# Kernel tuning notes

Hardware: AMD Instinct MI355X
Metric: run time of the kernel (lower is better)

## Reference

```python
import jax, jax.numpy as jnp
import numpy as np
from jax import lax

B, N, F = 64, 768, 256
P, T, K = 64, 16, 3  # per_lead, after_lead, kernel_size


def setup_inputs() -> dict:
    key = jax.random.key(0)
    k1, k2, k3, k4, k5 = jax.random.split(key, 5)
    x = jax.random.normal(k1, (B, N, F), dtype=jnp.float32)
    adj = jax.random.uniform(k2, (B, N, N), dtype=jnp.float32)
    fan_in = P * 1 * K
    bound = 1.0 / np.sqrt(fan_in)
    conv_w = jax.random.uniform(k3, (T, P, 1, K), minval=-bound, maxval=bound, dtype=jnp.float32)
    conv_b = jax.random.uniform(k4, (T,), minval=-bound, maxval=bound, dtype=jnp.float32)
    re_param = jax.random.normal(k5, (K, 1), dtype=jnp.float32)
    return {"x": x, "adj": adj, "conv_w": conv_w, "conv_b": conv_b, "re_param": re_param}


def reference(x, adj, conv_w, conv_b, re_param):
    b, n, f = x.shape
    t, p, _, k = conv_w.shape
    L = n // p  # number of leads
    # feature pooling: [B, P, L, F] -conv(1,k)-> [B, T, L, F]
    x4 = x.reshape(b, p, L, f)
    pad = (k - 1) // 2
    y = lax.conv_general_dilated(
        x4, conv_w, window_strides=(1, 1), padding=[(0, 0), (pad, pad)],
        dimension_numbers=("NCHW", "OIHW", "NCHW"))
    y = y + conv_b[None, :, None, None]
    pooled_x = y.reshape(b, t * L, f)
    # assignment matrix s = conv_w @ re_param  -> [T, P]
    s = jnp.einsum("tpik,kj->tp", conv_w, re_param)
    # block-diagonal coarsening: for every (lead_i, lead_j) block do s @ A_ij @ s^T
    adj5 = adj.reshape(b, L, p, L, p)
    pooled = jnp.einsum("tp,blpmq,uq->bltmu", s, adj5, s)
    pooled_adj = pooled.reshape(b, L * t, L * t)
    return pooled_x, pooled_adj
```

## Files before the change

### kernel.cpp

```cpp
#include <hip/hip_runtime.h>

#define B_ 64
#define N_ 768
#define F_ 256
#define P_ 64
#define T_ 16
#define K_ 3
#define L_ 12
#define TSTR 772

__global__ __launch_bounds__(256) void fused_pool_kernel(
    const float* __restrict__ x, const float* __restrict__ adj,
    const float* __restrict__ conv_w, const float* __restrict__ conv_b,
    const float* __restrict__ re_param,
    float* __restrict__ out_x, float* __restrict__ out_adj)
{
    __shared__ float sT[P_][T_];
    __shared__ float tmp[T_][TSTR];

    const int g  = blockIdx.x;
    const int Lg = (g & 7) * 192 + (g >> 3);
    const int b  = Lg / 24;
    const int r  = Lg % 24;
    const int tid = threadIdx.x;

    if (r >= L_) {
        const int l = r - L_;
        const int f = tid;
        const float* xb = x + (size_t)b * N_ * F_ + (size_t)l * F_;

        float acc[T_];
        #pragma unroll
        for (int t = 0; t < T_; ++t) acc[t] = conv_b[t];

        for (int p0 = 0; p0 < P_; p0 += 2) {
            float xm[2], x0[2], xp[2];
            #pragma unroll
            for (int rr = 0; rr < 2; ++rr) {
                const float* row = xb + (size_t)(p0 + rr) * (L_ * F_);
                xm[rr] = (f > 0)      ? row[f - 1] : 0.f;
                x0[rr] = row[f];
                xp[rr] = (f < F_ - 1) ? row[f + 1] : 0.f;
            }
            #pragma unroll
            for (int rr = 0; rr < 2; ++rr) {
                const float* wp = conv_w + (p0 + rr) * K_;
                #pragma unroll
                for (int t = 0; t < T_; ++t) {
                    const float w0 = wp[t * (P_ * K_) + 0];
                    const float w1 = wp[t * (P_ * K_) + 1];
                    const float w2 = wp[t * (P_ * K_) + 2];
                    acc[t] = fmaf(xm[rr], w0, fmaf(x0[rr], w1, fmaf(xp[rr], w2, acc[t])));
                }
            }
        }
        float* ob = out_x + (size_t)b * (T_ * L_) * F_ + f;
        #pragma unroll
        for (int t = 0; t < T_; ++t)
            ob[(size_t)(t * L_ + l) * F_] = acc[t];
        return;
    }

    const int l = r;

    const float r0 = re_param[0], r1 = re_param[1], r2 = re_param[2];
    for (int j = tid; j < P_ * T_; j += 256) {
        const int p = j >> 4, t = j & 15;
        const float* wv = conv_w + (size_t)t * (P_ * K_) + (size_t)p * K_;
        sT[p][t] = wv[0] * r0 + wv[1] * r1 + wv[2] * r2;
    }
    __syncthreads();

    float acc[T_][3];
    #pragma unroll
    for (int t = 0; t < T_; ++t)
        #pragma unroll
        for (int c = 0; c < 3; ++c) acc[t][c] = 0.f;

    const float* ab = adj + (size_t)b * N_ * N_ + (size_t)(l * P_) * N_ + tid;
    for (int p0 = 0; p0 < P_; p0 += 8) {
        float a[8][3];
        #pragma unroll
        for (int rr = 0; rr < 8; ++rr) {
            const float* row = ab + (size_t)(p0 + rr) * N_;
            a[rr][0] = row[0];
            a[rr][1] = row[256];
            a[rr][2] = row[512];
        }
        #pragma unroll
        for (int rr = 0; rr < 8; ++rr) {
            #pragma unroll
            for (int j = 0; j < 4; ++j) {
                const float4 sv = *(const float4*)&sT[p0 + rr][4 * j];
                acc[4*j+0][0] = fmaf(sv.x, a[rr][0], acc[4*j+0][0]);
                acc[4*j+0][1] = fmaf(sv.x, a[rr][1], acc[4*j+0][1]);
                acc[4*j+0][2] = fmaf(sv.x, a[rr][2], acc[4*j+0][2]);
                acc[4*j+1][0] = fmaf(sv.y, a[rr][0], acc[4*j+1][0]);
                acc[4*j+1][1] = fmaf(sv.y, a[rr][1], acc[4*j+1][1]);
                acc[4*j+1][2] = fmaf(sv.y, a[rr][2], acc[4*j+1][2]);
                acc[4*j+2][0] = fmaf(sv.z, a[rr][0], acc[4*j+2][0]);
                acc[4*j+2][1] = fmaf(sv.z, a[rr][1], acc[4*j+2][1]);
                acc[4*j+2][2] = fmaf(sv.z, a[rr][2], acc[4*j+2][2]);
                acc[4*j+3][0] = fmaf(sv.w, a[rr][0], acc[4*j+3][0]);
                acc[4*j+3][1] = fmaf(sv.w, a[rr][1], acc[4*j+3][1]);
                acc[4*j+3][2] = fmaf(sv.w, a[rr][2], acc[4*j+3][2]);
            }
        }
    }
    #pragma unroll
    for (int t = 0; t < T_; ++t) {
        tmp[t][tid]       = acc[t][0];
        tmp[t][tid + 256] = acc[t][1];
        tmp[t][tid + 512] = acc[t][2];
    }
    __syncthreads();

    const int t = tid >> 4, u = tid & 15;
    float sum[L_];
    #pragma unroll
    for (int m = 0; m < L_; ++m) sum[m] = 0.f;

    for (int q4 = 0; q4 < P_; q4 += 4) {
        const float s0 = sT[q4 + 0][u];
        const float s1 = sT[q4 + 1][u];
        const float s2 = sT[q4 + 2][u];
        const float s3 = sT[q4 + 3][u];
        #pragma unroll
        for (int m = 0; m < L_; ++m) {
            const float4 tv = *(const float4*)&tmp[t][m * P_ + q4];
            sum[m] = fmaf(tv.x, s0, fmaf(tv.y, s1, fmaf(tv.z, s2, fmaf(tv.w, s3, sum[m]))));
        }
    }

    float* ob = out_adj + (size_t)b * (L_ * T_) * (L_ * T_)
                        + (size_t)(l * T_ + t) * (L_ * T_) + u;
    #pragma unroll
    for (int m = 0; m < L_; ++m)
        ob[m * T_] = sum[m];
}

extern "C" void kernel_launch(void* const* d_in, const int* in_sizes, int n_in,
                              void* d_out, int out_size, void* d_ws, size_t ws_size,
                              hipStream_t stream) {
    (void)in_sizes; (void)n_in; (void)out_size; (void)d_ws; (void)ws_size;
    const float* x        = (const float*)d_in[0];
    const float* adj      = (const float*)d_in[1];
    const float* conv_w   = (const float*)d_in[2];
    const float* conv_b   = (const float*)d_in[3];
    const float* re_param = (const float*)d_in[4];

    float* pooled_x   = (float*)d_out;
    float* pooled_adj = (float*)d_out + (size_t)B_ * (T_ * L_) * F_;

    fused_pool_kernel<<<B_ * L_ * 2, 256, 0, stream>>>(
        x, adj, conv_w, conv_b, re_param, pooled_x, pooled_adj);
}
```

Before: 87.14 us.

## Precompute assignment matrix in separate kernel and split adj work across T halves

A small pre-kernel now computes s = conv_w·re_param once into workspace, in both layouts, so blocks no longer each recompute it. The adj blocks use 192 threads with float4 loads and split the 16 output rows into two halves of 8. That doubles the adj block count and halves shared memory and registers per block. The x-conv blocks drop to 192 threads with a strided loop over features and a deeper unroll. The cost is an extra kernel launch, each adj tile being read twice (once per T half), and the second stage running on only 128 of the 192 threads.

```diff
diff --git a/kernel.cpp b/kernel.cpp
--- a/kernel.cpp
+++ b/kernel.cpp
@@ -9,140 +9,151 @@
 #define L_ 12
 #define TSTR 772
 
-__global__ __launch_bounds__(256) void fused_pool_kernel(
+
+__global__ void compute_s_kernel(const float* __restrict__ conv_w,
+                                 const float* __restrict__ re_param,
+                                 float* __restrict__ ws) {
+    const int j = blockIdx.x * 256 + threadIdx.x;
+    if (j < P_ * T_) {
+        const int p = j >> 4, t = j & 15;
+        const float* w = conv_w + (size_t)t * (P_ * K_) + (size_t)p * K_;
+        const float s = w[0] * re_param[0] + w[1] * re_param[1] + w[2] * re_param[2];
+        ws[p * T_ + t] = s;
+        ws[1024 + t * P_ + p] = s;
+    }
+}
+
+__global__ __launch_bounds__(192, 5) void fused_kernel(
     const float* __restrict__ x, const float* __restrict__ adj,
     const float* __restrict__ conv_w, const float* __restrict__ conv_b,
-    const float* __restrict__ re_param,
+    const float* __restrict__ ws,
     float* __restrict__ out_x, float* __restrict__ out_adj)
 {
-    __shared__ float sT[P_][T_];
-    __shared__ float tmp[T_][TSTR];
+    __shared__ float sS[P_][8];
+    __shared__ float tmp[8][TSTR];
 
-    const int g  = blockIdx.x;
-    const int Lg = (g & 7) * 192 + (g >> 3);
-    const int b  = Lg / 24;
-    const int r  = Lg % 24;
+    const int g = blockIdx.x;
     const int tid = threadIdx.x;
 
-    if (r >= L_) {
-        const int l = r - L_;
-        const int f = tid;
-        const float* xb = x + (size_t)b * N_ * F_ + (size_t)l * F_;
+    if (g < 1536) {
+        const int r  = g & 7;
+        const int h  = g >> 3;
+        const int tg = h & 1;
+        const int bl = r + 8 * (h >> 1);
+        const int b = bl / L_, l = bl % L_;
 
-        float acc[T_];
+        if (tid < 128) {
+            const int p = tid >> 1, hh = tid & 1;
+            const float4 v = *(const float4*)(ws + p * T_ + 8 * tg + 4 * hh);
+            *(float4*)&sS[p][4 * hh] = v;
+        }
+        __syncthreads();
+
+        const int c4 = tid;
+        const float* arow = adj + (size_t)bl * (P_ * N_) + 4 * c4;
+
+        float acc[8][4];
         #pragma unroll
-        for (int t = 0; t < T_; ++t) acc[t] = conv_b[t];
+        for (int j = 0; j < 8; ++j) {
+            acc[j][0] = 0.f; acc[j][1] = 0.f; acc[j][2] = 0.f; acc[j][3] = 0.f;
+        }
 
-        for (int p0 = 0; p0 < P_; p0 += 2) {
-            float xm[2], x0[2], xp[2];
+        for (int p0 = 0; p0 < P_; p0 += 8) {
+            float4 a[8];
             #pragma unroll
-            for (int rr = 0; rr < 2; ++rr) {
-                const float* row = xb + (size_t)(p0 + rr) * (L_ * F_);
-                xm[rr] = (f > 0)      ? row[f - 1] : 0.f;
-                x0[rr] = row[f];
-                xp[rr] = (f < F_ - 1) ? row[f + 1] : 0.f;
-            }
+            for (int rr = 0; rr < 8; ++rr)
+                a[rr] = *(const float4*)(arow + (size_t)(p0 + rr) * N_);
             #pragma unroll
-            for (int rr = 0; rr < 2; ++rr) {
-                const float* wp = conv_w + (p0 + rr) * K_;
-                #pragma unroll
-                for (int t = 0; t < T_; ++t) {
-                    const float w0 = wp[t * (P_ * K_) + 0];
-                    const float w1 = wp[t * (P_ * K_) + 1];
-                    const float w2 = wp[t * (P_ * K_) + 2];
-                    acc[t] = fmaf(xm[rr], w0, fmaf(x0[rr], w1, fmaf(xp[rr], w2, acc[t])));
-                }
+            for (int rr = 0; rr < 8; ++rr) {
+                const float4 s0 = *(const float4*)&sS[p0 + rr][0];
+                const float4 s1 = *(const float4*)&sS[p0 + rr][4];
+#define FMA4(J, SV) \
+    acc[J][0] = fmaf(SV, a[rr].x, acc[J][0]); \
+    acc[J][1] = fmaf(SV, a[rr].y, acc[J][1]); \
+    acc[J][2] = fmaf(SV, a[rr].z, acc[J][2]); \
+    acc[J][3] = fmaf(SV, a[rr].w, acc[J][3]);
+                FMA4(0, s0.x) FMA4(1, s0.y) FMA4(2, s0.z) FMA4(3, s0.w)
+                FMA4(4, s1.x) FMA4(5, s1.y) FMA4(6, s1.z) FMA4(7, s1.w)
+#undef FMA4
             }
         }
-        float* ob = out_x + (size_t)b * (T_ * L_) * F_ + f;
+
         #pragma unroll
-        for (int t = 0; t < T_; ++t)
-            ob[(size_t)(t * L_ + l) * F_] = acc[t];
+        for (int j = 0; j < 8; ++j) {
+            float4 v;
+            v.x = acc[j][0]; v.y = acc[j][1]; v.z = acc[j][2]; v.w = acc[j][3];
+            *(float4*)&tmp[j][4 * c4] = v;
+        }
+        __syncthreads();
+
+        if (tid < 128) {
+            const int j = tid >> 4, u = tid & 15;
+            float4 su[16];
+            #pragma unroll
+            for (int q4 = 0; q4 < 16; ++q4)
+                su[q4] = *(const float4*)(ws + 1024 + u * P_ + 4 * q4);
+
+            const int row = l * T_ + 8 * tg + j;
+            float* ob = out_adj + (size_t)b * (L_ * T_) * (L_ * T_)
+                                + (size_t)row * (L_ * T_) + u;
+            for (int m = 0; m < L_; ++m) {
+                float sum = 0.f;
+                #pragma unroll
+                for (int q4 = 0; q4 < 16; ++q4) {
+                    const float4 tv = *(const float4*)&tmp[j][m * P_ + 4 * q4];
+                    sum = fmaf(tv.x, su[q4].x, fmaf(tv.y, su[q4].y,
+                          fmaf(tv.z, su[q4].z, fmaf(tv.w, su[q4].w, sum))));
+                }
+                ob[m * T_] = sum;
+            }
+        }
         return;
     }
 
-    const int l = r;
+    const int bl = g - 1536;
+    const int b = bl / L_, l = bl % L_;
+    const float* xb = x + (size_t)b * N_ * F_ + (size_t)l * F_;
 
-    const float r0 = re_param[0], r1 = re_param[1], r2 = re_param[2];
-    for (int j = tid; j < P_ * T_; j += 256) {
-        const int p = j >> 4, t = j & 15;
-        const float* wv = conv_w + (size_t)t * (P_ * K_) + (size_t)p * K_;
-        sT[p][t] = wv[0] * r0 + wv[1] * r1 + wv[2] * r2;
-    }
-    __syncthreads();
+    for (int f0 = 0; f0 < F_; f0 += 192) {
+        const int f = f0 + tid;
+        if (f < F_) {
+            float acc[T_];
+            #pragma unroll
+            for (int t = 0; t < T_; ++t) acc[t] = conv_b[t];
 
-    float acc[T_][3];
-    #pragma unroll
-    for (int t = 0; t < T_; ++t)
-        #pragma unroll
-        for (int c = 0; c < 3; ++c) acc[t][c] = 0.f;
-
-    const float* ab = adj + (size_t)b * N_ * N_ + (size_t)(l * P_) * N_ + tid;
-    for (int p0 = 0; p0 < P_; p0 += 8) {
-        float a[8][3];
-        #pragma unroll
-        for (int rr = 0; rr < 8; ++rr) {
-            const float* row = ab + (size_t)(p0 + rr) * N_;
-            a[rr][0] = row[0];
-            a[rr][1] = row[256];
-            a[rr][2] = row[512];
-        }
-        #pragma unroll
-        for (int rr = 0; rr < 8; ++rr) {
+            for (int p0 = 0; p0 < P_; p0 += 4) {
+                float xm[4], x0[4], xp[4];
+                #pragma unroll
+                for (int rr = 0; rr < 4; ++rr) {
+                    const float* row = xb + (size_t)(p0 + rr) * (L_ * F_);
+                    xm[rr] = (f > 0)      ? row[f - 1] : 0.f;
+                    x0[rr] = row[f];
+                    xp[rr] = (f < F_ - 1) ? row[f + 1] : 0.f;
+                }
+                #pragma unroll
+                for (int rr = 0; rr < 4; ++rr) {
+                    const float* wp = conv_w + (p0 + rr) * K_;
+                    #pragma unroll
+                    for (int t = 0; t < T_; ++t) {
+                        const float w0 = wp[t * (P_ * K_) + 0];
+                        const float w1 = wp[t * (P_ * K_) + 1];
+                        const float w2 = wp[t * (P_ * K_) + 2];
+                        acc[t] = fmaf(xm[rr], w0, fmaf(x0[rr], w1, fmaf(xp[rr], w2, acc[t])));
+                    }
+                }
+            }
+            float* ob = out_x + (size_t)b * (T_ * L_) * F_ + f;
             #pragma unroll
-            for (int j = 0; j < 4; ++j) {
-                const float4 sv = *(const float4*)&sT[p0 + rr][4 * j];
-                acc[4*j+0][0] = fmaf(sv.x, a[rr][0], acc[4*j+0][0]);
-                acc[4*j+0][1] = fmaf(sv.x, a[rr][1], acc[4*j+0][1]);
-                acc[4*j+0][2] = fmaf(sv.x, a[rr][2], acc[4*j+0][2]);
-                acc[4*j+1][0] = fmaf(sv.y, a[rr][0], acc[4*j+1][0]);
-                acc[4*j+1][1] = fmaf(sv.y, a[rr][1], acc[4*j+1][1]);
-                acc[4*j+1][2] = fmaf(sv.y, a[rr][2], acc[4*j+1][2]);
-                acc[4*j+2][0] = fmaf(sv.z, a[rr][0], acc[4*j+2][0]);
-                acc[4*j+2][1] = fmaf(sv.z, a[rr][1], acc[4*j+2][1]);
-                acc[4*j+2][2] = fmaf(sv.z, a[rr][2], acc[4*j+2][2]);
-                acc[4*j+3][0] = fmaf(sv.w, a[rr][0], acc[4*j+3][0]);
-                acc[4*j+3][1] = fmaf(sv.w, a[rr][1], acc[4*j+3][1]);
-                acc[4*j+3][2] = fmaf(sv.w, a[rr][2], acc[4*j+3][2]);
-            }
+            for (int t = 0; t < T_; ++t)
+                ob[(size_t)(t * L_ + l) * F_] = acc[t];
         }
     }
-    #pragma unroll
-    for (int t = 0; t < T_; ++t) {
-        tmp[t][tid]       = acc[t][0];
-        tmp[t][tid + 256] = acc[t][1];
-        tmp[t][tid + 512] = acc[t][2];
-    }
-    __syncthreads();
-
-    const int t = tid >> 4, u = tid & 15;
-    float sum[L_];
-    #pragma unroll
-    for (int m = 0; m < L_; ++m) sum[m] = 0.f;
-
-    for (int q4 = 0; q4 < P_; q4 += 4) {
-        const float s0 = sT[q4 + 0][u];
-        const float s1 = sT[q4 + 1][u];
-        const float s2 = sT[q4 + 2][u];
-        const float s3 = sT[q4 + 3][u];
-        #pragma unroll
-        for (int m = 0; m < L_; ++m) {
-            const float4 tv = *(const float4*)&tmp[t][m * P_ + q4];
-            sum[m] = fmaf(tv.x, s0, fmaf(tv.y, s1, fmaf(tv.z, s2, fmaf(tv.w, s3, sum[m]))));
-        }
-    }
-
-    float* ob = out_adj + (size_t)b * (L_ * T_) * (L_ * T_)
-                        + (size_t)(l * T_ + t) * (L_ * T_) + u;
-    #pragma unroll
-    for (int m = 0; m < L_; ++m)
-        ob[m * T_] = sum[m];
 }
 
 extern "C" void kernel_launch(void* const* d_in, const int* in_sizes, int n_in,
                               void* d_out, int out_size, void* d_ws, size_t ws_size,
                               hipStream_t stream) {
-    (void)in_sizes; (void)n_in; (void)out_size; (void)d_ws; (void)ws_size;
+    (void)in_sizes; (void)n_in; (void)out_size; (void)ws_size;
     const float* x        = (const float*)d_in[0];
     const float* adj      = (const float*)d_in[1];
     const float* conv_w   = (const float*)d_in[2];
@@ -151,7 +162,9 @@
 
     float* pooled_x   = (float*)d_out;
     float* pooled_adj = (float*)d_out + (size_t)B_ * (T_ * L_) * F_;
+    float* ws         = (float*)d_ws;
 
-    fused_pool_kernel<<<B_ * L_ * 2, 256, 0, stream>>>(
-        x, adj, conv_w, conv_b, re_param, pooled_x, pooled_adj);
+    compute_s_kernel<<<4, 256, 0, stream>>>(conv_w, re_param, ws);
+    fused_kernel<<<1536 + 768, 192, 0, stream>>>(
+        x, adj, conv_w, conv_b, ws, pooled_x, pooled_adj);
 }
```

Result: slower. 100.4 us (+15.2%).
